# Kernel tuning notes

Measured on AMD Instinct MI355X. Metric: run time of the kernel, lower is better.

Reference implementation:

```python
import jax, jax.numpy as jnp
import numpy as np

ROI = (8, 8)          # local window (kh, kw)
H = 768
W = 768
C = ROI[0] * ROI[1]   # 64 channels == prod(roi), required by the local conv
N_LAYERS = 4          # n_decoder_layers
LN_EPS = 1e-6         # flax.linen.LayerNorm default


def setup_inputs() -> dict:
    key = jax.random.key(0)
    k0, k1, k2 = jax.random.split(key, 3)
    x = jax.random.normal(k0, (H, W, C), jnp.float32)  # post-FPN feature map
    Ws = jax.random.normal(k1, (N_LAYERS, C, C), jnp.float32) / np.float32(np.sqrt(C))
    bs = jnp.zeros((N_LAYERS, C), jnp.float32)
    ln_scale = jnp.ones((N_LAYERS, C), jnp.float32)
    ln_bias = jnp.zeros((N_LAYERS, C), jnp.float32)
    w_out = jax.random.normal(k2, (C, 1), jnp.float32) / np.float32(np.sqrt(C))
    b_out = jnp.zeros((1,), jnp.float32)
    return {"x": x, "Ws": Ws, "bs": bs, "ln_scale": ln_scale,
            "ln_bias": ln_bias, "w_out": w_out, "b_out": b_out}


def att(x, weights):
    # out[i,j,c] = sum_{di,dj} xpad[i+di, j+dj, c] * weights[i, j, di*kw+dj]
    # Equivalent to the original per-channel lax.scan over
    # conv_general_dilated_local (window ordering row-major, 'same' padding),
    # but batched over all C channels at once via shifted-slice accumulation
    # instead of materializing the (H, W, 64, C) patch tensor.
    kh, kw = ROI
    pt, pb = (kh - 1) // 2, kh - 1 - (kh - 1) // 2  # 'SAME' pad for even kernel: (3, 4)
    pl, pr = (kw - 1) // 2, kw - 1 - (kw - 1) // 2
    xpad = jnp.pad(x, ((pt, pb), (pl, pr), (0, 0)))

    def body(acc, k):
        di = k // kw
        dj = k % kw
        patch = jax.lax.dynamic_slice(xpad, (di, dj, 0), (H, W, C))
        return acc + patch * weights[:, :, k][:, :, None], None

    acc, _ = jax.lax.scan(body, jnp.zeros_like(x), jnp.arange(kh * kw))
    return acc


def layer_norm(x, scale, bias):
    mu = jnp.mean(x, axis=-1, keepdims=True)
    var = jnp.mean(jnp.square(x - mu), axis=-1, keepdims=True)
    return (x - mu) * jax.lax.rsqrt(var + LN_EPS) * scale + bias


def reference(x, Ws, bs, ln_scale, ln_bias, w_out, b_out):
    weights = jax.nn.sigmoid(x)            # spatially-varying local-conv weights
    x0 = att(x, weights)                   # (H, W, C)
    for i in range(N_LAYERS):              # MLP decoder stack
        x0 = jax.nn.relu(x0 @ Ws[i] + bs[i])
        x0 = layer_norm(x0, ln_scale[i], ln_bias[i])
    out = x0 @ w_out + b_out               # (H, W, 1)
    return (x0, out)
```

## Files before the change

### kernel.cpp

```cpp
#include <hip/hip_runtime.h>
#include <hip/hip_bf16.h>


#define HH 768
#define WW 768
#define HWPX (HH*WW)

typedef __attribute__((ext_vector_type(8))) short short8;
typedef __attribute__((ext_vector_type(8))) _Float16 half8;
typedef __attribute__((ext_vector_type(4))) float f32x4;
typedef __attribute__((ext_vector_type(16))) float f32x16;

union hcvt { _Float16 h; ushort u; };
__device__ __forceinline__ ushort f2h(float f) { hcvt c; c.h = (_Float16)f; return c.u; }
__device__ __forceinline__ float sigmoidf(float v) { return 1.f / (1.f + __expf(-v)); }

__device__ __forceinline__ int goff(int row, int g) {
  return (row << 8) + (((g & ~7) | ((g ^ row) & 7)) << 3);
}
__device__ __forceinline__ int eoff(int row, int k) {
  const int g = k >> 3;
  return (row << 8) + (((g & ~7) | ((g ^ row) & 7)) << 3) + (k & 7);
}

template<bool F16OUT>
__global__ __launch_bounds__(256, 2)
void att_k1(const float* __restrict__ x, void* __restrict__ attout) {
  __shared__ __align__(16) ushort Mb[64 * 256];
  __shared__ __align__(16) ushort Xb[64 * 256];
  const int tid = threadIdx.x;
  const int lane = tid & 63, w = tid >> 6;
  const int l15 = lane & 15, lg = lane >> 4;
  const int l31 = lane & 31, lh = lane >> 5;

  {
    const short8 z8 = {0,0,0,0,0,0,0,0};
    #pragma unroll
    for (int i = 0; i < 8; ++i)
      *reinterpret_cast<short8*>(&Mb[(tid + i * 256) * 8]) = z8;
  }

  const int b = blockIdx.x;
  const int tbase = (b & 7) * 1152 + (b >> 3) * 18;
  const int p  = w * 16 + l15;
  const int pr = p >> 3, pc = p & 7;
  const int cb = lg << 4;
  const int pb = w >> 1, cb2 = w & 1;

  float4 cv[4];
  float Rv[4][8];
  float Lv[4][8];
  short8 rs[4];

  auto issue_loads = [&](int ti, int tj, bool fresh) {
    {
      const float* cp = x + ((size_t)((ti + pr) * WW + (tj + pc)) << 6) + cb;
      #pragma unroll
      for (int qd = 0; qd < 4; ++qd)
        cv[qd] = *reinterpret_cast<const float4*>(cp + qd * 4);
    }
    #pragma unroll
    for (int i = 0; i < 4; ++i) {
      const int r = w + 4 * i;
      if (r < 15) {
        const int gr = min(max(ti + r - 3, 0), HH - 1);
        const float* rowp = x + ((size_t)gr * WW << 6) + lane;
        #pragma unroll
        for (int s = 0; s < 8; ++s) {
          const int gc = min(max(tj + 5 + s, 0), WW - 1);
          Rv[i][s] = rowp[(size_t)gc << 6];
        }
        if (fresh) {
          #pragma unroll
          for (int s = 0; s < 8; ++s) {
            const int gc = min(max(tj - 3 + s, 0), WW - 1);
            Lv[i][s] = rowp[(size_t)gc << 6];
          }
        }
      }
    }
  };

  auto write_lds = [&](int ti, int tj, bool fresh) {
    #pragma unroll
    for (int qd = 0; qd < 4; ++qd) {
      const float vs[4] = {cv[qd].x, cv[qd].y, cv[qd].z, cv[qd].w};
      #pragma unroll
      for (int j = 0; j < 4; ++j) {
        const int ch = cb + qd * 4 + j;
        const int k = ((pr + (ch >> 3)) << 4) | (pc + (ch & 7));
        Mb[eoff(p, k)] = f2h(sigmoidf(vs[j]));
      }
    }
    #pragma unroll
    for (int i = 0; i < 4; ++i) {
      const int r = w + 4 * i;
      if (r < 15) {
        const int gr = ti + r - 3;
        const bool rok = (unsigned)gr < (unsigned)HH;
        short8 left8;
        if (fresh) {
          #pragma unroll
          for (int s = 0; s < 8; ++s) {
            const int j = tj - 3 + s;
            const bool ok = rok && ((unsigned)j < (unsigned)WW);
            left8[s] = (short)f2h(ok ? Lv[i][s] : 0.f);
          }
        } else {
          left8 = rs[i];
        }
        short8 right8;
        #pragma unroll
        for (int s = 0; s < 8; ++s) {
          const int j = tj + 5 + s;
          const bool ok = rok && ((unsigned)j < (unsigned)WW);
          right8[s] = (short)f2h(ok ? Rv[i][s] : 0.f);
        }
        *reinterpret_cast<short8*>(&Xb[goff(lane, 2 * r)])     = left8;
        *reinterpret_cast<short8*>(&Xb[goff(lane, 2 * r + 1)]) = right8;
        rs[i] = right8;
      }
    }
  };

  f32x16 acc0, acc1;
  int pti = 0, ptj = 0;

  auto store_acc = [&](int ti, int tj) {
    #pragma unroll
    for (int reg = 0; reg < 16; ++reg) {
      const float v = acc0[reg] + acc1[reg];
      const int prow = (reg & 3) + 8 * (reg >> 2) + 4 * lh;
      const int p2 = pb * 32 + prow;
      const size_t gpx = (size_t)(ti + (p2 >> 3)) * WW + (tj + (p2 & 7));
      const int ch = cb2 * 32 + l31;
      if (F16OUT) ((ushort*)attout)[(gpx << 6) + ch] = f2h(v);
      else        ((float*)attout)[(gpx << 6) + ch] = v;
    }
  };

  issue_loads((tbase / 96) * 8, (tbase % 96) * 8, true);

  for (int t18 = 0; t18 < 18; ++t18) {
    const int tile = tbase + t18;
    const int ti = (tile / 96) * 8, tj = (tile % 96) * 8;
    const bool fresh = (t18 == 0) || (tj == 0);

    __syncthreads();
    write_lds(ti, tj, fresh);
    __syncthreads();

    if (t18 > 0) store_acc(pti, ptj);
    if (t18 < 17) {
      const int nt = tile + 1;
      issue_loads((nt / 96) * 8, (nt % 96) * 8, (nt % 96) == 0);
    }

    acc0 = (f32x16){0,0,0,0,0,0,0,0,0,0,0,0,0,0,0,0};
    acc1 = (f32x16){0,0,0,0,0,0,0,0,0,0,0,0,0,0,0,0};
    #pragma unroll
    for (int ks = 0; ks < 15; ++ks) {
      const int g = 2 * ks + lh;
      const half8 a  = *reinterpret_cast<const half8*>(&Mb[goff(pb * 32 + l31, g)]);
      const half8 bb = *reinterpret_cast<const half8*>(&Xb[goff(cb2 * 32 + l31, g)]);
      if (ks & 1) acc1 = __builtin_amdgcn_mfma_f32_32x32x16_f16(a, bb, acc1, 0, 0, 0);
      else        acc0 = __builtin_amdgcn_mfma_f32_32x32x16_f16(a, bb, acc0, 0, 0, 0);
    }
    pti = ti; ptj = tj;
  }
  store_acc(pti, ptj);
}

template<bool F16IN>
__global__ __launch_bounds__(512, 4)
void mlp_k2(const void* attv, const float* __restrict__ Ws,
            const float* __restrict__ bs, const float* __restrict__ lns,
            const float* __restrict__ lnb, const float* __restrict__ w_out,
            const float* __restrict__ b_out, float* x0_out,
            float* __restrict__ out1) {
  __shared__ __align__(16) ushort wt[4 * 64 * 64];
  __shared__ __align__(16) ushort act[8 * 1152];
  const int tid = threadIdx.x;
  const int lane = tid & 63, wid = tid >> 6;
  const int l15 = lane & 15, lg = lane >> 4;

  {
    const int row = tid >> 1;
    const int l = row >> 6, co = row & 63;
    const int ci0 = (tid & 1) << 5;
    const int base = row << 6;
    for (int q = 0; q < 32; ++q) {
      const int ci = ci0 + q;
      const float v = Ws[(((l << 6) + ci) << 6) + co];
      const int e = ((((ci >> 3) ^ co) & 7) << 3) | (ci & 7);
      wt[base + e] = f2h(v);
    }
  }
  float bias[4][4], sc[4][4], lbv[4][4];
  #pragma unroll
  for (int L = 0; L < 4; ++L)
    #pragma unroll
    for (int nb = 0; nb < 4; ++nb) {
      const int ch = (L << 6) + nb * 16 + l15;
      bias[L][nb] = bs[ch]; sc[L][nb] = lns[ch]; lbv[L][nb] = lnb[ch];
    }
  float wo[4];
  #pragma unroll
  for (int nb = 0; nb < 4; ++nb) wo[nb] = w_out[nb * 16 + l15];
  const float b0s = b_out[0];
  __syncthreads();

  ushort* const acth = act + wid * 1152;

  for (int it = 0; it < 18; ++it) {
    const int chunk = blockIdx.x + (it << 8);
    const int px_base = chunk * 128 + wid * 16;

    half8 a0, a1;
    if (F16IN) {
      const ushort* ap = (const ushort*)attv + ((size_t)(px_base + l15) << 6) + lg * 8;
      a0 = *reinterpret_cast<const half8*>(ap);
      a1 = *reinterpret_cast<const half8*>(ap + 32);
    } else {
      const float* ap = (const float*)attv + ((size_t)(px_base + l15) << 6) + lg * 8;
      const float4 f0 = *reinterpret_cast<const float4*>(ap);
      const float4 f1 = *reinterpret_cast<const float4*>(ap + 4);
      const float4 f2 = *reinterpret_cast<const float4*>(ap + 32);
      const float4 f3 = *reinterpret_cast<const float4*>(ap + 36);
      a0[0]=(_Float16)f0.x; a0[1]=(_Float16)f0.y; a0[2]=(_Float16)f0.z; a0[3]=(_Float16)f0.w;
      a0[4]=(_Float16)f1.x; a0[5]=(_Float16)f1.y; a0[6]=(_Float16)f1.z; a0[7]=(_Float16)f1.w;
      a1[0]=(_Float16)f2.x; a1[1]=(_Float16)f2.y; a1[2]=(_Float16)f2.z; a1[3]=(_Float16)f2.w;
      a1[4]=(_Float16)f3.x; a1[5]=(_Float16)f3.y; a1[6]=(_Float16)f3.z; a1[7]=(_Float16)f3.w;
    }

    float y[4][4];
    #pragma unroll
    for (int layer = 0; layer < 4; ++layer) {
      if (layer > 0) {
        a0 = *reinterpret_cast<const half8*>(&acth[l15 * 72 + lg * 8]);
        a1 = *reinterpret_cast<const half8*>(&acth[l15 * 72 + 32 + lg * 8]);
      }
      f32x4 z[4];
      #pragma unroll
      for (int nb = 0; nb < 4; ++nb) {
        const int co = nb * 16 + l15;
        const int wb = ((layer << 6) + co) << 6;
        const int e0 = (((lg    ) ^ co) & 7) << 3;
        const int e1 = (((lg + 4) ^ co) & 7) << 3;
        const half8 b0 = *reinterpret_cast<const half8*>(&wt[wb + e0]);
        const half8 b1 = *reinterpret_cast<const half8*>(&wt[wb + e1]);
        z[nb] = {0.f, 0.f, 0.f, 0.f};
        z[nb] = __builtin_amdgcn_mfma_f32_16x16x32_f16(a0, b0, z[nb], 0, 0, 0);
        z[nb] = __builtin_amdgcn_mfma_f32_16x16x32_f16(a1, b1, z[nb], 0, 0, 0);
      }
      #pragma unroll
      for (int reg = 0; reg < 4; ++reg) {
        float s = 0.f, ss = 0.f;
        #pragma unroll
        for (int nb = 0; nb < 4; ++nb) {
          float v = z[nb][reg] + bias[layer][nb];
          v = fmaxf(v, 0.f);
          y[reg][nb] = v;
          s += v; ss += v * v;
        }
        #pragma unroll
        for (int m = 1; m <= 8; m <<= 1) { s += __shfl_xor(s, m, 64); ss += __shfl_xor(ss, m, 64); }
        const float mu = s * 0.015625f;
        const float var = ss * 0.015625f - mu * mu;
        const float rstd = rsqrtf(var + 1e-6f);
        #pragma unroll
        for (int nb = 0; nb < 4; ++nb)
          y[reg][nb] = (y[reg][nb] - mu) * rstd * sc[layer][nb] + lbv[layer][nb];
      }
      if (layer < 3) {
        #pragma unroll
        for (int reg = 0; reg < 4; ++reg) {
          const int row = lg * 4 + reg;
          #pragma unroll
          for (int nb = 0; nb < 4; ++nb)
            acth[row * 72 + nb * 16 + l15] = f2h(y[reg][nb]);
        }
      }
    }

    #pragma unroll
    for (int reg = 0; reg < 4; ++reg) {
      const size_t pxg = (size_t)px_base + lg * 4 + reg;
      #pragma unroll
      for (int nb = 0; nb < 4; ++nb)
        x0_out[(pxg << 6) + nb * 16 + l15] = y[reg][nb];
      float part = y[reg][0] * wo[0] + y[reg][1] * wo[1] + y[reg][2] * wo[2] + y[reg][3] * wo[3];
      #pragma unroll
      for (int m = 1; m <= 8; m <<= 1) part += __shfl_xor(part, m, 64);
      if (l15 == 0) out1[pxg] = part + b0s;
    }
  }
}

extern "C" void kernel_launch(void* const* d_in, const int* in_sizes, int n_in,
                              void* d_out, int out_size, void* d_ws, size_t ws_size,
                              hipStream_t stream) {
  const float* x     = (const float*)d_in[0];
  const float* Ws    = (const float*)d_in[1];
  const float* bs    = (const float*)d_in[2];
  const float* lns   = (const float*)d_in[3];
  const float* lnbv  = (const float*)d_in[4];
  const float* w_out = (const float*)d_in[5];
  const float* b_out = (const float*)d_in[6];
  float* x0_out = (float*)d_out;
  float* out1   = x0_out + (size_t)HWPX * 64;

  if (ws_size >= (size_t)HWPX * 64 * sizeof(ushort)) {
    ushort* atth = (ushort*)d_ws;
    att_k1<true><<<512, 256, 0, stream>>>(x, atth);
    mlp_k2<true><<<256, 512, 0, stream>>>(atth, Ws, bs, lns, lnbv,
                                          w_out, b_out, x0_out, out1);
  } else {
    att_k1<false><<<512, 256, 0, stream>>>(x, d_out);
    mlp_k2<false><<<256, 512, 0, stream>>>(d_out, Ws, bs, lns, lnbv,
                                           w_out, b_out, x0_out, out1);
  }
}
```

Baseline: 195.7 us.

## Fold LayerNorm affine and bias into weights, switch MLP to 32x32 MFMA

A new prep kernel folds each layer's LayerNorm scale and shift, together with the linear bias, into the next layer's weight matrix. It also appends extra K columns holding the bias and a column sum, so bias and mean subtraction happen inside the MFMA through constant-one and -mu*rstd activation entries. The MLP kernel moves from 16x16x32 to 32x32x16 MFMA tiles with 32 pixels per wave, which cuts the LayerNorm cross-lane reduction to a single shuffle and allows vectorized x0 stores. The cost is an extra small launch, a fifth K-slice of MFMA work, fp16 rounding of the folded bias and mu terms, and lower occupancy (launch bounds drop from 4 to 2 blocks).

```diff
diff --git a/kernel.cpp b/kernel.cpp
--- a/kernel.cpp
+++ b/kernel.cpp
@@ -21,6 +21,27 @@
 __device__ __forceinline__ int eoff(int row, int k) {
   const int g = k >> 3;
   return (row << 8) + (((g & ~7) | ((g ^ row) & 7)) << 3) + (k & 7);
+}
+
+__global__ __launch_bounds__(256)
+void prep_wf(const float* __restrict__ Ws, const float* __restrict__ bs,
+             const float* __restrict__ lns, const float* __restrict__ lnb,
+             ushort* __restrict__ Wfg) {
+  const int L = threadIdx.x >> 6, co = threadIdx.x & 63;
+  float bias = bs[L * 64 + co];
+  float colsum = 0.f;
+  ushort* row = Wfg + (size_t)(L * 64 + co) * 80;
+  for (int ci = 0; ci < 64; ++ci) {
+    const float w = Ws[((L * 64 + ci) << 6) + co];
+    const float sc = (L > 0) ? lns[(L - 1) * 64 + ci] : 1.f;
+    const float wp = sc * w;
+    if (L > 0) bias += lnb[(L - 1) * 64 + ci] * w;
+    colsum += wp;
+    row[ci] = f2h(wp);
+  }
+  row[64] = f2h(bias);
+  row[65] = f2h(colsum);
+  for (int q = 66; q < 80; ++q) row[q] = 0;
 }
 
 template<bool F16OUT>
@@ -171,129 +192,144 @@
   store_acc(pti, ptj);
 }
 
+__device__ __forceinline__ float zsel(const f32x16& z0, const f32x16& z1, int nb, int idx) {
+  return nb ? z1[idx] : z0[idx];
+}
+
 template<bool F16IN>
-__global__ __launch_bounds__(512, 4)
-void mlp_k2(const void* attv, const float* __restrict__ Ws,
-            const float* __restrict__ bs, const float* __restrict__ lns,
-            const float* __restrict__ lnb, const float* __restrict__ w_out,
-            const float* __restrict__ b_out, float* x0_out,
-            float* __restrict__ out1) {
-  __shared__ __align__(16) ushort wt[4 * 64 * 64];
-  __shared__ __align__(16) ushort act[8 * 1152];
+__global__ __launch_bounds__(512, 2)
+void mlp_k2(const void* attv, const ushort* __restrict__ Wfg,
+            const float* __restrict__ lns, const float* __restrict__ lnb,
+            const float* __restrict__ w_out, const float* __restrict__ b_out,
+            float* x0_out, float* __restrict__ out1) {
+  __shared__ __align__(16) ushort wt[4 * 64 * 88];
+  __shared__ __align__(16) ushort act[8][32 * 88];
+  __shared__ __align__(16) ushort kpat[16];
   const int tid = threadIdx.x;
   const int lane = tid & 63, wid = tid >> 6;
-  const int l15 = lane & 15, lg = lane >> 4;
-
-  {
-    const int row = tid >> 1;
-    const int l = row >> 6, co = row & 63;
-    const int ci0 = (tid & 1) << 5;
-    const int base = row << 6;
-    for (int q = 0; q < 32; ++q) {
-      const int ci = ci0 + q;
-      const float v = Ws[(((l << 6) + ci) << 6) + co];
-      const int e = ((((ci >> 3) ^ co) & 7) << 3) | (ci & 7);
-      wt[base + e] = f2h(v);
-    }
-  }
-  float bias[4][4], sc[4][4], lbv[4][4];
+  const int l31 = lane & 31, lh = lane >> 5;
+
+  for (int idx = tid; idx < 4 * 64 * 10; idx += 512) {
+    const int row = idx / 10, q = idx - row * 10;
+    *reinterpret_cast<uint4*>(&wt[row * 88 + q * 8]) =
+        *reinterpret_cast<const uint4*>(&Wfg[(size_t)row * 80 + q * 8]);
+  }
+  for (int idx = tid; idx < 256; idx += 512) {
+    ushort* rp = &act[idx >> 5][(idx & 31) * 88];
+    for (int q = 64; q < 88; ++q) rp[q] = 0;
+    rp[64] = 0x3C00;
+  }
+  if (tid < 16) kpat[tid] = (tid == 0) ? (ushort)0x3C00 : (ushort)0;
+
+  float sc3[2][4][4], lb3[2][4][4], wo3[2][4][4];
   #pragma unroll
-  for (int L = 0; L < 4; ++L)
-    #pragma unroll
-    for (int nb = 0; nb < 4; ++nb) {
-      const int ch = (L << 6) + nb * 16 + l15;
-      bias[L][nb] = bs[ch]; sc[L][nb] = lns[ch]; lbv[L][nb] = lnb[ch];
-    }
-  float wo[4];
-  #pragma unroll
-  for (int nb = 0; nb < 4; ++nb) wo[nb] = w_out[nb * 16 + l15];
+  for (int nb = 0; nb < 2; ++nb)
+    #pragma unroll
+    for (int hi = 0; hi < 4; ++hi)
+      #pragma unroll
+      for (int j = 0; j < 4; ++j) {
+        const int ch = nb * 32 + hi * 8 + lh * 4 + j;
+        sc3[nb][hi][j] = lns[192 + ch];
+        lb3[nb][hi][j] = lnb[192 + ch];
+        wo3[nb][hi][j] = w_out[ch];
+      }
   const float b0s = b_out[0];
   __syncthreads();
 
-  ushort* const acth = act + wid * 1152;
-
-  for (int it = 0; it < 18; ++it) {
-    const int chunk = blockIdx.x + (it << 8);
-    const int px_base = chunk * 128 + wid * 16;
-
-    half8 a0, a1;
+  ushort* const myact = act[wid];
+
+  for (int it = 0; it < 9; ++it) {
+    const int px = ((it * 256 + (int)blockIdx.x) * 8 + wid) * 32 + l31;
+
+    half8 bfr[5];
     if (F16IN) {
-      const ushort* ap = (const ushort*)attv + ((size_t)(px_base + l15) << 6) + lg * 8;
-      a0 = *reinterpret_cast<const half8*>(ap);
-      a1 = *reinterpret_cast<const half8*>(ap + 32);
+      const ushort* ap = (const ushort*)attv + ((size_t)px << 6) + lh * 8;
+      #pragma unroll
+      for (int g = 0; g < 4; ++g)
+        bfr[g] = *reinterpret_cast<const half8*>(ap + g * 16);
     } else {
-      const float* ap = (const float*)attv + ((size_t)(px_base + l15) << 6) + lg * 8;
-      const float4 f0 = *reinterpret_cast<const float4*>(ap);
-      const float4 f1 = *reinterpret_cast<const float4*>(ap + 4);
-      const float4 f2 = *reinterpret_cast<const float4*>(ap + 32);
-      const float4 f3 = *reinterpret_cast<const float4*>(ap + 36);
-      a0[0]=(_Float16)f0.x; a0[1]=(_Float16)f0.y; a0[2]=(_Float16)f0.z; a0[3]=(_Float16)f0.w;
-      a0[4]=(_Float16)f1.x; a0[5]=(_Float16)f1.y; a0[6]=(_Float16)f1.z; a0[7]=(_Float16)f1.w;
-      a1[0]=(_Float16)f2.x; a1[1]=(_Float16)f2.y; a1[2]=(_Float16)f2.z; a1[3]=(_Float16)f2.w;
-      a1[4]=(_Float16)f3.x; a1[5]=(_Float16)f3.y; a1[6]=(_Float16)f3.z; a1[7]=(_Float16)f3.w;
-    }
-
-    float y[4][4];
-    #pragma unroll
-    for (int layer = 0; layer < 4; ++layer) {
-      if (layer > 0) {
-        a0 = *reinterpret_cast<const half8*>(&acth[l15 * 72 + lg * 8]);
-        a1 = *reinterpret_cast<const half8*>(&acth[l15 * 72 + 32 + lg * 8]);
-      }
-      f32x4 z[4];
-      #pragma unroll
-      for (int nb = 0; nb < 4; ++nb) {
-        const int co = nb * 16 + l15;
-        const int wb = ((layer << 6) + co) << 6;
-        const int e0 = (((lg    ) ^ co) & 7) << 3;
-        const int e1 = (((lg + 4) ^ co) & 7) << 3;
-        const half8 b0 = *reinterpret_cast<const half8*>(&wt[wb + e0]);
-        const half8 b1 = *reinterpret_cast<const half8*>(&wt[wb + e1]);
-        z[nb] = {0.f, 0.f, 0.f, 0.f};
-        z[nb] = __builtin_amdgcn_mfma_f32_16x16x32_f16(a0, b0, z[nb], 0, 0, 0);
-        z[nb] = __builtin_amdgcn_mfma_f32_16x16x32_f16(a1, b1, z[nb], 0, 0, 0);
-      }
-      #pragma unroll
-      for (int reg = 0; reg < 4; ++reg) {
-        float s = 0.f, ss = 0.f;
-        #pragma unroll
-        for (int nb = 0; nb < 4; ++nb) {
-          float v = z[nb][reg] + bias[layer][nb];
-          v = fmaxf(v, 0.f);
-          y[reg][nb] = v;
-          s += v; ss += v * v;
-        }
-        #pragma unroll
-        for (int m = 1; m <= 8; m <<= 1) { s += __shfl_xor(s, m, 64); ss += __shfl_xor(ss, m, 64); }
-        const float mu = s * 0.015625f;
-        const float var = ss * 0.015625f - mu * mu;
-        const float rstd = rsqrtf(var + 1e-6f);
-        #pragma unroll
-        for (int nb = 0; nb < 4; ++nb)
-          y[reg][nb] = (y[reg][nb] - mu) * rstd * sc[layer][nb] + lbv[layer][nb];
-      }
-      if (layer < 3) {
-        #pragma unroll
-        for (int reg = 0; reg < 4; ++reg) {
-          const int row = lg * 4 + reg;
+      const float* ap = (const float*)attv + ((size_t)px << 6) + lh * 8;
+      #pragma unroll
+      for (int g = 0; g < 4; ++g) {
+        const float4 fa = *reinterpret_cast<const float4*>(ap + g * 16);
+        const float4 fb = *reinterpret_cast<const float4*>(ap + g * 16 + 4);
+        half8 h;
+        h[0]=(_Float16)fa.x; h[1]=(_Float16)fa.y; h[2]=(_Float16)fa.z; h[3]=(_Float16)fa.w;
+        h[4]=(_Float16)fb.x; h[5]=(_Float16)fb.y; h[6]=(_Float16)fb.z; h[7]=(_Float16)fb.w;
+        bfr[g] = h;
+      }
+    }
+    bfr[4] = *reinterpret_cast<const half8*>(&kpat[lh * 8]);
+
+    f32x16 z0, z1;
+    float mu = 0.f, rstd = 1.f;
+    #pragma unroll
+    for (int L = 0; L < 4; ++L) {
+      if (L > 0) {
+        #pragma unroll
+        for (int g = 0; g < 5; ++g)
+          bfr[g] = *reinterpret_cast<const half8*>(&myact[l31 * 88 + g * 16 + lh * 8]);
+      }
+      z0 = (f32x16){0,0,0,0,0,0,0,0,0,0,0,0,0,0,0,0};
+      z1 = (f32x16){0,0,0,0,0,0,0,0,0,0,0,0,0,0,0,0};
+      #pragma unroll
+      for (int g = 0; g < 5; ++g) {
+        const half8 a0 = *reinterpret_cast<const half8*>(&wt[(L * 64      + l31) * 88 + g * 16 + lh * 8]);
+        const half8 a1 = *reinterpret_cast<const half8*>(&wt[(L * 64 + 32 + l31) * 88 + g * 16 + lh * 8]);
+        z0 = __builtin_amdgcn_mfma_f32_32x32x16_f16(a0, bfr[g], z0, 0, 0, 0);
+        z1 = __builtin_amdgcn_mfma_f32_32x32x16_f16(a1, bfr[g], z1, 0, 0, 0);
+      }
+      float sp[4] = {0.f, 0.f, 0.f, 0.f}, qp[4] = {0.f, 0.f, 0.f, 0.f};
+      #pragma unroll
+      for (int r = 0; r < 16; ++r) {
+        const float v0 = fmaxf(z0[r], 0.f); z0[r] = v0;
+        const float v1 = fmaxf(z1[r], 0.f); z1[r] = v1;
+        sp[r & 3] += v0 + v1;
+        qp[r & 3] += v0 * v0 + v1 * v1;
+      }
+      float s = (sp[0] + sp[1]) + (sp[2] + sp[3]);
+      float qq = (qp[0] + qp[1]) + (qp[2] + qp[3]);
+      s  += __shfl_xor(s, 32, 64);
+      qq += __shfl_xor(qq, 32, 64);
+      mu = s * 0.015625f;
+      const float var = qq * 0.015625f - mu * mu;
+      rstd = rsqrtf(var + 1e-6f);
+      if (L < 3) {
+        #pragma unroll
+        for (int nb = 0; nb < 2; ++nb)
           #pragma unroll
-          for (int nb = 0; nb < 4; ++nb)
-            acth[row * 72 + nb * 16 + l15] = f2h(y[reg][nb]);
-        }
-      }
-    }
-
-    #pragma unroll
-    for (int reg = 0; reg < 4; ++reg) {
-      const size_t pxg = (size_t)px_base + lg * 4 + reg;
-      #pragma unroll
-      for (int nb = 0; nb < 4; ++nb)
-        x0_out[(pxg << 6) + nb * 16 + l15] = y[reg][nb];
-      float part = y[reg][0] * wo[0] + y[reg][1] * wo[1] + y[reg][2] * wo[2] + y[reg][3] * wo[3];
-      #pragma unroll
-      for (int m = 1; m <= 8; m <<= 1) part += __shfl_xor(part, m, 64);
-      if (l15 == 0) out1[pxg] = part + b0s;
-    }
+          for (int hi = 0; hi < 4; ++hi) {
+            ushort4 pk;
+            pk.x = f2h(rstd * zsel(z0, z1, nb, hi * 4 + 0));
+            pk.y = f2h(rstd * zsel(z0, z1, nb, hi * 4 + 1));
+            pk.z = f2h(rstd * zsel(z0, z1, nb, hi * 4 + 2));
+            pk.w = f2h(rstd * zsel(z0, z1, nb, hi * 4 + 3));
+            *reinterpret_cast<ushort4*>(&myact[l31 * 88 + nb * 32 + hi * 8 + lh * 4]) = pk;
+          }
+        if (lh == 0) myact[l31 * 88 + 65] = f2h(-(mu * rstd));
+      }
+    }
+
+    const float t = mu * rstd;
+    float part0 = 0.f, part1 = 0.f;
+    #pragma unroll
+    for (int nb = 0; nb < 2; ++nb)
+      #pragma unroll
+      for (int hi = 0; hi < 4; ++hi) {
+        f32x4 yv;
+        #pragma unroll
+        for (int j = 0; j < 4; ++j) {
+          const float v = zsel(z0, z1, nb, hi * 4 + j);
+          const float y = v * (rstd * sc3[nb][hi][j]) + (lb3[nb][hi][j] - t * sc3[nb][hi][j]);
+          yv[j] = y;
+          if (j & 1) part1 += y * wo3[nb][hi][j];
+          else       part0 += y * wo3[nb][hi][j];
+        }
+        *reinterpret_cast<f32x4*>(&x0_out[((size_t)px << 6) + nb * 32 + hi * 8 + lh * 4]) = yv;
+      }
+    float part = part0 + part1;
+    part += __shfl_xor(part, 32, 64);
+    if (lh == 0) out1[px] = part + b0s;
   }
 }
 
@@ -310,14 +346,19 @@
   float* x0_out = (float*)d_out;
   float* out1   = x0_out + (size_t)HWPX * 64;
 
-  if (ws_size >= (size_t)HWPX * 64 * sizeof(ushort)) {
+  const size_t attBytes = (size_t)HWPX * 64 * sizeof(ushort);
+  if (ws_size >= attBytes + 65536) {
     ushort* atth = (ushort*)d_ws;
+    ushort* Wfg  = (ushort*)((char*)d_ws + attBytes);
+    prep_wf<<<1, 256, 0, stream>>>(Ws, bs, lns, lnbv, Wfg);
     att_k1<true><<<512, 256, 0, stream>>>(x, atth);
-    mlp_k2<true><<<256, 512, 0, stream>>>(atth, Ws, bs, lns, lnbv,
+    mlp_k2<true><<<256, 512, 0, stream>>>(atth, Wfg, lns, lnbv,
                                           w_out, b_out, x0_out, out1);
   } else {
+    ushort* Wfg = (ushort*)d_ws;
+    prep_wf<<<1, 256, 0, stream>>>(Ws, bs, lns, lnbv, Wfg);
     att_k1<false><<<512, 256, 0, stream>>>(x, d_out);
-    mlp_k2<false><<<256, 512, 0, stream>>>(d_out, Ws, bs, lns, lnbv,
+    mlp_k2<false><<<256, 512, 0, stream>>>(d_out, Wfg, lns, lnbv,
                                            w_out, b_out, x0_out, out1);
   }
 }
```

Result: faster. 187.7 us (-4.1%).
